# Kernel optimization log

Hardware: AMD Instinct MI355X
Metric: run time of the kernel (lower is better)

Reference implementation:

```python
import jax, jax.numpy as jnp
import numpy as np

# dims: B batch, N nodes, F in-feats, H time window, K Cheb order, G out-feats, C classes
B, N, F, H, K, G, C = 32, 16384, 1, 15, 25, 64, 6
E = N * 32  # edges


def setup_inputs() -> dict:
    key = jax.random.key(0)
    ks = jax.random.split(key, 8)
    x = jax.random.normal(ks[0], (B, N, F, H), jnp.float32)
    edge_src = jax.random.randint(ks[1], (E,), 0, N, jnp.int32)
    edge_dst = jax.random.randint(ks[2], (E,), 0, N, jnp.int32)
    # precomputed scaled-Laplacian edge weights (as in ChebConv norm)
    edge_weight = jax.random.uniform(ks[3], (E,), jnp.float32, minval=-0.1, maxval=0.1)
    W = jax.random.normal(ks[4], (K, H, F, G), jnp.float32) * 0.05   # Cheb time-conv weight
    b_conv = jnp.zeros((G,), jnp.float32)
    W_fc = jax.random.normal(ks[5], (C, N * G), jnp.float32) * 0.01  # torch Linear layout [out,in]
    b_fc = jnp.zeros((C,), jnp.float32)
    return dict(x=x, edge_weight=edge_weight, W=W, b_conv=b_conv,
                W_fc=W_fc, b_fc=b_fc, edge_src=edge_src, edge_dst=edge_dst)


def _spmm(edge_src, edge_dst, edge_weight, X):
    # sparse L @ X ; X: [N, D]  ->  y[i] = sum_{e: src=i} w_e * X[dst_e]
    return jax.ops.segment_sum(edge_weight[:, None] * X[edge_dst], edge_src, num_segments=N)


def reference(x, edge_weight, W, b_conv, W_fc, b_fc, edge_src, edge_dst):
    # Chebyshev recursion over the graph, joint contraction over time window and features
    X0 = jnp.transpose(x, (1, 0, 2, 3)).reshape(N, B * F * H)  # [N, B*F*H]

    def contract(Xk, Wk):
        # Xk: [N, B*F*H], Wk: [H, F, G] -> [B, N, G]
        return jnp.einsum('nbfh,hfg->bng', Xk.reshape(N, B, F, H), Wk)

    out = contract(X0, W[0])
    X1 = _spmm(edge_src, edge_dst, edge_weight, X0)
    out = out + contract(X1, W[1])
    Xkm2, Xkm1 = X0, X1
    for k in range(2, K):  # fixed K=25, structural loop
        Xk = 2.0 * _spmm(edge_src, edge_dst, edge_weight, Xkm1) - Xkm2
        out = out + contract(Xk, W[k])
        Xkm2, Xkm1 = Xkm1, Xk
    out = out + b_conv                         # [B, N, G]
    h = jax.nn.relu(out).reshape(B, N * G)     # x.view(B, -1)
    logits = h @ W_fc.T + b_fc                 # fc1
    return jax.nn.log_softmax(logits, axis=1)
```

## Files before the change

### kernel.cpp

```cpp
#include <hip/hip_runtime.h>
#include <hip/hip_bf16.h>
#include <math.h>

#define NN 16384
#define BB 32
#define HH 15
#define KK 25
#define GG 64
#define CC 6
#define EE (NN * 32)
#define NG ((size_t)NN * GG)
#define PSTRIDE 8192

typedef unsigned int u32;
typedef unsigned short u16;
typedef __attribute__((ext_vector_type(8))) short bf16x8;
typedef __attribute__((ext_vector_type(4))) float f32x4;
typedef __attribute__((ext_vector_type(4))) u32 u32x4;


__global__ void init_counts(int* __restrict__ cnt) {
    int t = blockIdx.x * 256 + threadIdx.x;
    if (t < NN) cnt[t] = 0;
}

__global__ void hist_kernel(const int* __restrict__ src, int* __restrict__ cnt) {
    int e = blockIdx.x * 256 + threadIdx.x;
    if (e < EE) atomicAdd(&cnt[src[e]], 1);
}

__global__ __launch_bounds__(1024) void scan_kernel(const int* __restrict__ cnt,
                                                    int* __restrict__ rowptr,
                                                    int* __restrict__ cursor) {
    __shared__ int sums[1024];
    int t = threadIdx.x;
    int base = t * 16;
    int local[16];
    int s = 0;
#pragma unroll
    for (int i = 0; i < 16; ++i) { local[i] = s; s += cnt[base + i]; }
    sums[t] = s;
    __syncthreads();
    for (int off = 1; off < 1024; off <<= 1) {
        int v = (t >= off) ? sums[t - off] : 0;
        __syncthreads();
        sums[t] += v;
        __syncthreads();
    }
    int prefix = (t == 0) ? 0 : sums[t - 1];
#pragma unroll
    for (int i = 0; i < 16; ++i) {
        int rp = prefix + local[i];
        rowptr[base + i] = rp;
        cursor[base + i] = rp;
    }
    if (t == 1023) rowptr[NN] = sums[1023];
}

__global__ void scatter_kernel(const int* __restrict__ src, const int* __restrict__ dst,
                               const float* __restrict__ w, int* __restrict__ cursor,
                               int* __restrict__ col, float* __restrict__ wgt) {
    int e = blockIdx.x * 256 + threadIdx.x;
    if (e < EE) {
        int pos = atomicAdd(&cursor[src[e]], 1);
        col[pos] = dst[e];
        wgt[pos] = w[e];
    }
}


__device__ __forceinline__ u16 f2bf(float f) {
    __hip_bfloat16 b = __float2bfloat16(f);
    return *reinterpret_cast<u16*>(&b);
}
__device__ __forceinline__ float bflo(u32 d) { return __uint_as_float(d << 16); }
__device__ __forceinline__ float bfhi(u32 d) { return __uint_as_float(d & 0xffff0000u); }


__global__ void prep_wbf(const float* __restrict__ W, u16* __restrict__ WbfT) {
    int t = blockIdx.x * 256 + threadIdx.x;
    if (t >= GG * 416) return;
    int g = t / 416;
    int f = t % 416;
    int k = f >> 4;
    int h = f & 15;
    float v = (k < KK && h < HH) ? W[(k * HH + h) * GG + g] : 0.f;
    WbfT[(size_t)g * 416 + f] = f2bf(v);
}


template<int BCH>
__global__ void transpose_bf(const float* __restrict__ x, u32* __restrict__ X0, int b0) {
    constexpr int CW = BCH * 8;
    int t = blockIdx.x * 256 + threadIdx.x;
    int n = t / CW;
    int j = t % CW;
    int bb = j >> 3;
    int h0 = (j & 7) * 2;
    const float* xb = x + ((size_t)(b0 + bb) * NN + n) * HH;
    float lo = xb[h0];
    float hi = (h0 + 1 < HH) ? xb[h0 + 1] : 0.f;
    X0[t] = (u32)f2bf(lo) | ((u32)f2bf(hi) << 16);
}


__global__ __launch_bounds__(256) void spmm_bf32(
    const int* __restrict__ rowptr, const int* __restrict__ col, const float* __restrict__ wgt,
    const u32* __restrict__ Xin, const u32* __restrict__ Xprev, u32* __restrict__ Xout,
    float alpha, float beta)
{
    int qc   = threadIdx.x >> 6;
    int lane = threadIdx.x & 63;
    int n = blockIdx.x;
    int e0 = rowptr[n], e1 = rowptr[n + 1];
    int grp = lane >> 4;
    int m16 = lane & 15;
    const u32* xq = Xin + (size_t)qc * 64 + (size_t)m16 * 4;

    float al[4] = {0.f,0.f,0.f,0.f}, ah[4] = {0.f,0.f,0.f,0.f};
    float bl[4] = {0.f,0.f,0.f,0.f}, bh[4] = {0.f,0.f,0.f,0.f};

    for (int base = e0; base < e1; base += 64) {
        int cnt = e1 - base;
        if (cnt > 64) cnt = 64;
        int cv = 0; float wv = 0.f;
        if (lane < cnt) { cv = col[base + lane]; wv = wgt[base + lane]; }
        int j = 0;
        for (; j + 8 <= cnt; j += 8) {
            int   iA = __shfl(cv, j + grp);
            float wA = __shfl(wv, j + grp);
            int   iB = __shfl(cv, j + 4 + grp);
            float wB = __shfl(wv, j + 4 + grp);
            u32x4 dA = *(const u32x4*)(xq + (size_t)iA * 256);
            u32x4 dB = *(const u32x4*)(xq + (size_t)iB * 256);
#pragma unroll
            for (int i = 0; i < 4; ++i) {
                al[i] = fmaf(wA, bflo(dA[i]), al[i]);
                ah[i] = fmaf(wA, bfhi(dA[i]), ah[i]);
                bl[i] = fmaf(wB, bflo(dB[i]), bl[i]);
                bh[i] = fmaf(wB, bfhi(dB[i]), bh[i]);
            }
        }
        for (; j < cnt; j += 4) {
            int   iA = __shfl(cv, j + grp);
            float wA = __shfl(wv, j + grp);
            u32x4 dA = *(const u32x4*)(xq + (size_t)iA * 256);
#pragma unroll
            for (int i = 0; i < 4; ++i) {
                al[i] = fmaf(wA, bflo(dA[i]), al[i]);
                ah[i] = fmaf(wA, bfhi(dA[i]), ah[i]);
            }
        }
    }

#pragma unroll
    for (int i = 0; i < 4; ++i) { al[i] += bl[i]; ah[i] += bh[i]; }
#pragma unroll
    for (int off = 16; off < 64; off <<= 1)
#pragma unroll
        for (int i = 0; i < 4; ++i) {
            al[i] += __shfl_xor(al[i], off);
            ah[i] += __shfl_xor(ah[i], off);
        }

    if (grp == 0) {
        size_t o = (size_t)n * 256 + (size_t)qc * 64 + (size_t)m16 * 4;
        u32x4 dp = {0,0,0,0};
        if (beta != 0.f) dp = *(const u32x4*)(Xprev + o);
        u32x4 r;
#pragma unroll
        for (int i = 0; i < 4; ++i) {
            float rl = alpha * al[i];
            float rh = alpha * ah[i];
            if (beta != 0.f) {
                rl = fmaf(beta, bflo(dp[i]), rl);
                rh = fmaf(beta, bfhi(dp[i]), rh);
            }
            r[i] = (u32)f2bf(rl) | ((u32)f2bf(rh) << 16);
        }
        *(u32x4*)(Xout + o) = r;
    }
}


__global__ __launch_bounds__(256) void spmm_bf8(
    const int* __restrict__ rowptr, const int* __restrict__ col, const float* __restrict__ wgt,
    const u32* __restrict__ Xin, const u32* __restrict__ Xprev, u32* __restrict__ Xout,
    float alpha, float beta)
{
    int sub  = threadIdx.x >> 6;
    int lane = threadIdx.x & 63;
    int n = blockIdx.x * 4 + sub;
    int e0 = rowptr[n], e1 = rowptr[n + 1];
    int grp = lane >> 4;
    int m16 = lane & 15;

    float al[4] = {0.f,0.f,0.f,0.f}, ah[4] = {0.f,0.f,0.f,0.f};
    float bl[4] = {0.f,0.f,0.f,0.f}, bh[4] = {0.f,0.f,0.f,0.f};

    for (int base = e0; base < e1; base += 64) {
        int cnt = e1 - base;
        if (cnt > 64) cnt = 64;
        int cv = 0; float wv = 0.f;
        if (lane < cnt) { cv = col[base + lane]; wv = wgt[base + lane]; }
        int j = 0;
        for (; j + 8 <= cnt; j += 8) {
            int   iA = __shfl(cv, j + grp);
            float wA = __shfl(wv, j + grp);
            int   iB = __shfl(cv, j + 4 + grp);
            float wB = __shfl(wv, j + 4 + grp);
            u32x4 dA = *(const u32x4*)(Xin + (size_t)iA * 64 + m16 * 4);
            u32x4 dB = *(const u32x4*)(Xin + (size_t)iB * 64 + m16 * 4);
#pragma unroll
            for (int i = 0; i < 4; ++i) {
                al[i] = fmaf(wA, bflo(dA[i]), al[i]);
                ah[i] = fmaf(wA, bfhi(dA[i]), ah[i]);
                bl[i] = fmaf(wB, bflo(dB[i]), bl[i]);
                bh[i] = fmaf(wB, bfhi(dB[i]), bh[i]);
            }
        }
        for (; j < cnt; j += 4) {
            int   iA = __shfl(cv, j + grp);
            float wA = __shfl(wv, j + grp);
            u32x4 dA = *(const u32x4*)(Xin + (size_t)iA * 64 + m16 * 4);
#pragma unroll
            for (int i = 0; i < 4; ++i) {
                al[i] = fmaf(wA, bflo(dA[i]), al[i]);
                ah[i] = fmaf(wA, bfhi(dA[i]), ah[i]);
            }
        }
    }

#pragma unroll
    for (int i = 0; i < 4; ++i) { al[i] += bl[i]; ah[i] += bh[i]; }
#pragma unroll
    for (int off = 16; off < 64; off <<= 1)
#pragma unroll
        for (int i = 0; i < 4; ++i) {
            al[i] += __shfl_xor(al[i], off);
            ah[i] += __shfl_xor(ah[i], off);
        }

    if (grp == 0) {
        size_t o = (size_t)n * 64 + (size_t)m16 * 4;
        u32x4 dp = {0,0,0,0};
        if (beta != 0.f) dp = *(const u32x4*)(Xprev + o);
        u32x4 r;
#pragma unroll
        for (int i = 0; i < 4; ++i) {
            float rl = alpha * al[i];
            float rh = alpha * ah[i];
            if (beta != 0.f) {
                rl = fmaf(beta, bflo(dp[i]), rl);
                rh = fmaf(beta, bfhi(dp[i]), rh);
            }
            r[i] = (u32)f2bf(rl) | ((u32)f2bf(rh) << 16);
        }
        *(u32x4*)(Xout + o) = r;
    }
}


__global__ __launch_bounds__(256) void spmm_bf4(
    const int* __restrict__ rowptr, const int* __restrict__ col, const float* __restrict__ wgt,
    const u32* __restrict__ Xin, const u32* __restrict__ Xprev, u32* __restrict__ Xout,
    float alpha, float beta)
{
    int sub  = threadIdx.x >> 6;
    int lane = threadIdx.x & 63;
    int n = blockIdx.x * 4 + sub;
    int e0 = rowptr[n], e1 = rowptr[n + 1];
    int grp = lane >> 3;
    int m8  = lane & 7;

    float al[4] = {0.f,0.f,0.f,0.f}, ah[4] = {0.f,0.f,0.f,0.f};
    float bl[4] = {0.f,0.f,0.f,0.f}, bh[4] = {0.f,0.f,0.f,0.f};

    for (int base = e0; base < e1; base += 64) {
        int cnt = e1 - base;
        if (cnt > 64) cnt = 64;
        int cv = 0; float wv = 0.f;
        if (lane < cnt) { cv = col[base + lane]; wv = wgt[base + lane]; }
        int j = 0;
        for (; j + 16 <= cnt; j += 16) {
            int   iA = __shfl(cv, j + grp);
            float wA = __shfl(wv, j + grp);
            int   iB = __shfl(cv, j + 8 + grp);
            float wB = __shfl(wv, j + 8 + grp);
            u32x4 dA = *(const u32x4*)(Xin + (size_t)iA * 32 + m8 * 4);
            u32x4 dB = *(const u32x4*)(Xin + (size_t)iB * 32 + m8 * 4);
#pragma unroll
            for (int i = 0; i < 4; ++i) {
                al[i] = fmaf(wA, bflo(dA[i]), al[i]);
                ah[i] = fmaf(wA, bfhi(dA[i]), ah[i]);
                bl[i] = fmaf(wB, bflo(dB[i]), bl[i]);
                bh[i] = fmaf(wB, bfhi(dB[i]), bh[i]);
            }
        }
        for (; j < cnt; j += 8) {
            int   iA = __shfl(cv, j + grp);
            float wA = __shfl(wv, j + grp);
            u32x4 dA = *(const u32x4*)(Xin + (size_t)iA * 32 + m8 * 4);
#pragma unroll
            for (int i = 0; i < 4; ++i) {
                al[i] = fmaf(wA, bflo(dA[i]), al[i]);
                ah[i] = fmaf(wA, bfhi(dA[i]), ah[i]);
            }
        }
    }

#pragma unroll
    for (int i = 0; i < 4; ++i) { al[i] += bl[i]; ah[i] += bh[i]; }
#pragma unroll
    for (int off = 8; off < 64; off <<= 1)
#pragma unroll
        for (int i = 0; i < 4; ++i) {
            al[i] += __shfl_xor(al[i], off);
            ah[i] += __shfl_xor(ah[i], off);
        }

    if (grp == 0) {
        size_t o = (size_t)n * 32 + (size_t)m8 * 4;
        u32x4 dp = {0,0,0,0};
        if (beta != 0.f) dp = *(const u32x4*)(Xprev + o);
        u32x4 r;
#pragma unroll
        for (int i = 0; i < 4; ++i) {
            float rl = alpha * al[i];
            float rh = alpha * ah[i];
            if (beta != 0.f) {
                rl = fmaf(beta, bflo(dp[i]), rl);
                rh = fmaf(beta, bfhi(dp[i]), rh);
            }
            r[i] = (u32)f2bf(rl) | ((u32)f2bf(rh) << 16);
        }
        *(u32x4*)(Xout + o) = r;
    }
}


template<int BCH>
__global__ __launch_bounds__(256) void spmm_bf(
    const int* __restrict__ rowptr, const int* __restrict__ col, const float* __restrict__ wgt,
    const u32* __restrict__ Xin, const u32* __restrict__ Xprev, u32* __restrict__ Xout,
    float alpha, float beta)
{
    constexpr int C  = BCH * 16;
    int sub  = threadIdx.x >> 6;
    int lane = threadIdx.x & 63;
    int n = blockIdx.x * 4 + sub;
    int e0 = rowptr[n], e1 = rowptr[n + 1];

    int c = lane;
    const u16* XinU  = (const u16*)Xin;
    const u16* XprevU= (const u16*)Xprev;
    u16* XoutU = (u16*)Xout;
    float a0=0.f,a1=0.f,a2=0.f,a3=0.f;
    bool act = (c < C);
    for (int base = e0; base < e1; base += 64) {
        int cnt = e1 - base;
        if (cnt > 64) cnt = 64;
        int cv = 0; float wv = 0.f;
        if (lane < cnt) { cv = col[base + lane]; wv = wgt[base + lane]; }
        int j = 0;
        for (; j + 4 <= cnt; j += 4) {
            int i0 = __builtin_amdgcn_readlane(cv, j);
            int i1 = __builtin_amdgcn_readlane(cv, j + 1);
            int i2 = __builtin_amdgcn_readlane(cv, j + 2);
            int i3 = __builtin_amdgcn_readlane(cv, j + 3);
            float w0 = __int_as_float(__builtin_amdgcn_readlane(__float_as_int(wv), j));
            float w1 = __int_as_float(__builtin_amdgcn_readlane(__float_as_int(wv), j + 1));
            float w2 = __int_as_float(__builtin_amdgcn_readlane(__float_as_int(wv), j + 2));
            float w3 = __int_as_float(__builtin_amdgcn_readlane(__float_as_int(wv), j + 3));
            if (act) {
                float x0 = __uint_as_float((u32)XinU[(size_t)i0 * C + c] << 16);
                float x1 = __uint_as_float((u32)XinU[(size_t)i1 * C + c] << 16);
                float x2 = __uint_as_float((u32)XinU[(size_t)i2 * C + c] << 16);
                float x3 = __uint_as_float((u32)XinU[(size_t)i3 * C + c] << 16);
                a0 = fmaf(w0, x0, a0);
                a1 = fmaf(w1, x1, a1);
                a2 = fmaf(w2, x2, a2);
                a3 = fmaf(w3, x3, a3);
            }
        }
        for (; j < cnt; ++j) {
            int i0 = __builtin_amdgcn_readlane(cv, j);
            float w0 = __int_as_float(__builtin_amdgcn_readlane(__float_as_int(wv), j));
            if (act) a0 = fmaf(w0, __uint_as_float((u32)XinU[(size_t)i0 * C + c] << 16), a0);
        }
    }
    if (act) {
        float r = alpha * ((a0 + a1) + (a2 + a3));
        size_t o = (size_t)n * C + c;
        if (beta != 0.f)
            r = fmaf(beta, __uint_as_float((u32)XprevU[o] << 16), r);
        XoutU[o] = f2bf(r);
    }
}


__global__ __launch_bounds__(256) void final4_32(
    const u32* __restrict__ Xall, const u16* __restrict__ WbfT,
    const float* __restrict__ b_conv, const float* __restrict__ Wfc,
    float* __restrict__ partials)
{
    constexpr int SLICE_DW = NN * 256;
    __shared__ float sred[2][32 * CC];
    int tid  = threadIdx.x;
    int wid  = tid >> 6;
    int lane = tid & 63;
    int q = lane >> 4;
    int m = lane & 15;
    int r0 = (blockIdx.x * 4 + wid) * 16;
    int r  = r0 + m;

    f32x4 acc0 = {0.f,0.f,0.f,0.f}, acc1 = {0.f,0.f,0.f,0.f};
    f32x4 acc2 = {0.f,0.f,0.f,0.f}, acc3 = {0.f,0.f,0.f,0.f};

    const u32* abase = Xall + (size_t)r * 8 + (size_t)(q & 1) * 4;
    const u16* bbase = WbfT + (size_t)m * 416 + q * 8;

#pragma unroll
    for (int s = 0; s < 13; ++s) {
        int ks = 2 * s + (q >> 1);
        bf16x8 af = {0,0,0,0,0,0,0,0};
        if (s < 12 || q < 2)
            af = *(const bf16x8*)(abase + (size_t)ks * SLICE_DW);
        bf16x8 bf0 = *(const bf16x8*)(bbase + (size_t)0 * 16 * 416 + s * 32);
        bf16x8 bf1 = *(const bf16x8*)(bbase + (size_t)1 * 16 * 416 + s * 32);
        bf16x8 bf2 = *(const bf16x8*)(bbase + (size_t)2 * 16 * 416 + s * 32);
        bf16x8 bf3 = *(const bf16x8*)(bbase + (size_t)3 * 16 * 416 + s * 32);
        acc0 = __builtin_amdgcn_mfma_f32_16x16x32_bf16(af, bf0, acc0, 0, 0, 0);
        acc1 = __builtin_amdgcn_mfma_f32_16x16x32_bf16(af, bf1, acc1, 0, 0, 0);
        acc2 = __builtin_amdgcn_mfma_f32_16x16x32_bf16(af, bf2, acc2, 0, 0, 0);
        acc3 = __builtin_amdgcn_mfma_f32_16x16x32_bf16(af, bf3, acc3, 0, 0, 0);
    }

    float part[4][CC];
#pragma unroll
    for (int i = 0; i < 4; ++i)
#pragma unroll
        for (int c = 0; c < CC; ++c) part[i][c] = 0.f;

#pragma unroll
    for (int gt = 0; gt < 4; ++gt) {
        f32x4 a = (gt == 0) ? acc0 : (gt == 1) ? acc1 : (gt == 2) ? acc2 : acc3;
        float bias = b_conv[gt * 16 + m];
#pragma unroll
        for (int i = 0; i < 4; ++i) {
            int rr = r0 + q * 4 + i;
            int nrow = rr >> 5;
            float hv = fmaxf(a[i] + bias, 0.f);
#pragma unroll
            for (int c = 0; c < CC; ++c)
                part[i][c] = fmaf(hv,
                    Wfc[(size_t)c * NG + (size_t)nrow * GG + gt * 16 + m], part[i][c]);
        }
    }

#pragma unroll
    for (int o = 1; o < 16; o <<= 1)
#pragma unroll
        for (int i = 0; i < 4; ++i)
#pragma unroll
            for (int c = 0; c < CC; ++c)
                part[i][c] += __shfl_xor(part[i][c], o);

    if (m == 0) {
        int node = wid >> 1;
        int bbb  = (wid & 1) * 16;
#pragma unroll
        for (int i = 0; i < 4; ++i)
#pragma unroll
            for (int c = 0; c < CC; ++c)
                sred[node][(bbb + q * 4 + i) * CC + c] = part[i][c];
    }
    __syncthreads();
    if (tid < 32 * CC) {
        float s2 = sred[0][tid] + sred[1][tid];
        int bb = tid / CC;
        int c  = tid % CC;
        partials[((size_t)bb * CC + c) * PSTRIDE + blockIdx.x] = s2;
    }
}


template<int BCH>
__global__ __launch_bounds__(256) void final4_t(
    const u32* __restrict__ Xall, const u16* __restrict__ WbfT,
    const float* __restrict__ b_conv, const float* __restrict__ Wfc,
    float* __restrict__ partials, int b0)
{
    constexpr int SLICE_DW = NN * BCH * 8;
    __shared__ float sred[4][BCH * CC];
    int tid  = threadIdx.x;
    int wid  = tid >> 6;
    int lane = tid & 63;
    int q = lane >> 4;
    int m = lane & 15;
    int r0 = (blockIdx.x * 4 + wid) * 16;
    int r  = r0 + m;

    f32x4 acc0 = {0.f,0.f,0.f,0.f}, acc1 = {0.f,0.f,0.f,0.f};
    f32x4 acc2 = {0.f,0.f,0.f,0.f}, acc3 = {0.f,0.f,0.f,0.f};

    const u32* abase = Xall + (size_t)r * 8 + (size_t)(q & 1) * 4;
    const u16* bbase = WbfT + (size_t)m * 416 + q * 8;

#pragma unroll
    for (int s = 0; s < 13; ++s) {
        int ks = 2 * s + (q >> 1);
        bf16x8 af = {0,0,0,0,0,0,0,0};
        if (s < 12 || q < 2)
            af = *(const bf16x8*)(abase + (size_t)ks * SLICE_DW);
        bf16x8 bf0 = *(const bf16x8*)(bbase + (size_t)0 * 16 * 416 + s * 32);
        bf16x8 bf1 = *(const bf16x8*)(bbase + (size_t)1 * 16 * 416 + s * 32);
        bf16x8 bf2 = *(const bf16x8*)(bbase + (size_t)2 * 16 * 416 + s * 32);
        bf16x8 bf3 = *(const bf16x8*)(bbase + (size_t)3 * 16 * 416 + s * 32);
        acc0 = __builtin_amdgcn_mfma_f32_16x16x32_bf16(af, bf0, acc0, 0, 0, 0);
        acc1 = __builtin_amdgcn_mfma_f32_16x16x32_bf16(af, bf1, acc1, 0, 0, 0);
        acc2 = __builtin_amdgcn_mfma_f32_16x16x32_bf16(af, bf2, acc2, 0, 0, 0);
        acc3 = __builtin_amdgcn_mfma_f32_16x16x32_bf16(af, bf3, acc3, 0, 0, 0);
    }

    float part[4][CC];
#pragma unroll
    for (int i = 0; i < 4; ++i)
#pragma unroll
        for (int c = 0; c < CC; ++c) part[i][c] = 0.f;

#pragma unroll
    for (int gt = 0; gt < 4; ++gt) {
        f32x4 a = (gt == 0) ? acc0 : (gt == 1) ? acc1 : (gt == 2) ? acc2 : acc3;
        float bias = b_conv[gt * 16 + m];
#pragma unroll
        for (int i = 0; i < 4; ++i) {
            int rr = r0 + q * 4 + i;
            int nrow = rr / BCH;
            float hv = fmaxf(a[i] + bias, 0.f);
#pragma unroll
            for (int c = 0; c < CC; ++c)
                part[i][c] = fmaf(hv,
                    Wfc[(size_t)c * NG + (size_t)nrow * GG + gt * 16 + m], part[i][c]);
        }
    }

#pragma unroll
    for (int o = 1; o < 16; o <<= 1)
#pragma unroll
        for (int i = 0; i < 4; ++i)
#pragma unroll
            for (int c = 0; c < CC; ++c)
                part[i][c] += __shfl_xor(part[i][c], o);

    if constexpr (BCH == 8) {
#pragma unroll
        for (int i = 0; i < 4; ++i)
#pragma unroll
            for (int c = 0; c < CC; ++c)
                part[i][c] += __shfl_xor(part[i][c], 32);
        if (m == 0 && q < 2) {
#pragma unroll
            for (int i = 0; i < 4; ++i)
#pragma unroll
                for (int c = 0; c < CC; ++c)
                    sred[wid][(q * 4 + i) * CC + c] = part[i][c];
        }
    } else {
#pragma unroll
        for (int o = 16; o < 64; o <<= 1)
#pragma unroll
            for (int i = 0; i < 4; ++i)
#pragma unroll
                for (int c = 0; c < CC; ++c)
                    part[i][c] += __shfl_xor(part[i][c], o);
        if (lane == 0) {
#pragma unroll
            for (int i = 0; i < 4; ++i)
#pragma unroll
                for (int c = 0; c < CC; ++c)
                    sred[wid][i * CC + c] = part[i][c];
        }
    }
    __syncthreads();
    if (tid < BCH * CC) {
        float s4 = sred[0][tid] + sred[1][tid] + sred[2][tid] + sred[3][tid];
        int bb = tid / CC;
        int c  = tid % CC;
        partials[((size_t)(b0 + bb) * CC + c) * PSTRIDE + blockIdx.x] = s4;
    }
}


template<int BCH>
__global__ __launch_bounds__(256) void final3_t(
    const u32* __restrict__ Xall, const float* __restrict__ W,
    const float* __restrict__ b_conv, const float* __restrict__ Wfc,
    float* __restrict__ partials, int b0)
{
    constexpr int CW = BCH * 8;
    __shared__ float sred[4][BCH * CC];
    int g   = threadIdx.x & 63;
    int nlu = __builtin_amdgcn_readfirstlane((int)threadIdx.x) >> 6;
    int n   = blockIdx.x * 4 + nlu;

    float acc[BCH];
#pragma unroll
    for (int bb = 0; bb < BCH; ++bb) acc[bb] = 0.f;

    for (int k = 0; k < KK; ++k) {
        const u32* __restrict__ xrow = Xall + ((size_t)k * NN + n) * CW;
        const float* __restrict__ Wk = W + k * (HH * GG);
        float wreg[HH];
#pragma unroll
        for (int h = 0; h < HH; ++h) wreg[h] = Wk[h * GG + g];
#pragma unroll
        for (int bb = 0; bb < BCH; ++bb) {
            float a = acc[bb];
#pragma unroll
            for (int p = 0; p < 8; ++p) {
                u32 d = xrow[bb * 8 + p];
                a = fmaf(bflo(d), wreg[2 * p], a);
                if (p < 7) a = fmaf(bfhi(d), wreg[2 * p + 1], a);
            }
            acc[bb] = a;
        }
    }

    float bias = b_conv[g];
    float wv[CC];
#pragma unroll
    for (int c = 0; c < CC; ++c)
        wv[c] = Wfc[(size_t)c * NG + (size_t)n * GG + g];

#pragma unroll
    for (int bb = 0; bb < BCH; ++bb) {
        float hv = fmaxf(acc[bb] + bias, 0.f);
#pragma unroll
        for (int c = 0; c < CC; ++c) {
            float s = hv * wv[c];
#pragma unroll
            for (int off = 1; off < 64; off <<= 1) s += __shfl_xor(s, off);
            if (g == 0) sred[nlu][bb * CC + c] = s;
        }
    }
    __syncthreads();
    if (threadIdx.x < BCH * CC) {
        float s = sred[0][threadIdx.x] + sred[1][threadIdx.x]
                + sred[2][threadIdx.x] + sred[3][threadIdx.x];
        int bb = threadIdx.x / CC;
        int c  = threadIdx.x % CC;
        partials[((size_t)(b0 + bb) * CC + c) * PSTRIDE + blockIdx.x] = s;
    }
}


__global__ __launch_bounds__(256) void reduce_logits(const float* __restrict__ partials,
                                                     float* __restrict__ logits, int nblk) {
    int idx = blockIdx.x;
    const float* p = partials + (size_t)idx * PSTRIDE;
    float s = 0.f;
    for (int i = threadIdx.x; i < nblk; i += 256) s += p[i];
#pragma unroll
    for (int off = 1; off < 64; off <<= 1) s += __shfl_xor(s, off);
    __shared__ float sr[4];
    if ((threadIdx.x & 63) == 0) sr[threadIdx.x >> 6] = s;
    __syncthreads();
    if (threadIdx.x == 0) logits[idx] = sr[0] + sr[1] + sr[2] + sr[3];
}


__global__ void lsm_kernel(const float* __restrict__ logits, const float* __restrict__ b_fc,
                           float* __restrict__ out) {
    int b = threadIdx.x;
    if (b >= BB) return;
    float v[CC];
    float m = -1e30f;
#pragma unroll
    for (int c = 0; c < CC; ++c) {
        v[c] = logits[b * CC + c] + b_fc[c];
        m = fmaxf(m, v[c]);
    }
    float s = 0.f;
#pragma unroll
    for (int c = 0; c < CC; ++c) s += expf(v[c] - m);
    float ls = m + logf(s);
#pragma unroll
    for (int c = 0; c < CC; ++c) out[b * CC + c] = v[c] - ls;
}

__global__ void sentinel_kernel(float* __restrict__ out) {
    int t = threadIdx.x;
    if (t < BB * CC) out[t] = -12345.f;
}


template<int BCH>
static void run_passes(const float* x, const float* W, const u16* WbfT,
                       const float* bconv, const float* Wfc,
                       const int* rowptr, const int* col, const float* wgt,
                       u32* Xall, float* partials, hipStream_t stream)
{
    constexpr int CW = BCH * 8;
    const size_t slice = (size_t)NN * CW;

    for (int p = 0; p < BB / BCH; ++p) {
        int b0 = p * BCH;
        transpose_bf<BCH><<<(NN * CW) / 256, 256, 0, stream>>>(x, Xall, b0);
        if constexpr (BCH == 32) {
            spmm_bf32<<<NN, 256, 0, stream>>>(
                rowptr, col, wgt, Xall, Xall, Xall + slice, 1.f, 0.f);
            for (int k = 2; k < KK; ++k) {
                spmm_bf32<<<NN, 256, 0, stream>>>(
                    rowptr, col, wgt,
                    Xall + (size_t)(k - 1) * slice,
                    Xall + (size_t)(k - 2) * slice,
                    Xall + (size_t)k * slice, 2.f, -1.f);
            }
            final4_32<<<NN * 32 / 64, 256, 0, stream>>>(Xall, WbfT, bconv, Wfc, partials);
        } else if constexpr (BCH == 8) {
            spmm_bf8<<<NN / 4, 256, 0, stream>>>(
                rowptr, col, wgt, Xall, Xall, Xall + slice, 1.f, 0.f);
            for (int k = 2; k < KK; ++k) {
                spmm_bf8<<<NN / 4, 256, 0, stream>>>(
                    rowptr, col, wgt,
                    Xall + (size_t)(k - 1) * slice,
                    Xall + (size_t)(k - 2) * slice,
                    Xall + (size_t)k * slice, 2.f, -1.f);
            }
            final4_t<8><<<NN * 8 / 64, 256, 0, stream>>>(Xall, WbfT, bconv, Wfc, partials, b0);
        } else if constexpr (BCH == 4) {
            spmm_bf4<<<NN / 4, 256, 0, stream>>>(
                rowptr, col, wgt, Xall, Xall, Xall + slice, 1.f, 0.f);
            for (int k = 2; k < KK; ++k) {
                spmm_bf4<<<NN / 4, 256, 0, stream>>>(
                    rowptr, col, wgt,
                    Xall + (size_t)(k - 1) * slice,
                    Xall + (size_t)(k - 2) * slice,
                    Xall + (size_t)k * slice, 2.f, -1.f);
            }
            final4_t<4><<<NN * 4 / 64, 256, 0, stream>>>(Xall, WbfT, bconv, Wfc, partials, b0);
        } else {
            spmm_bf<BCH><<<NN / 4, 256, 0, stream>>>(
                rowptr, col, wgt, Xall, Xall, Xall + slice, 1.f, 0.f);
            for (int k = 2; k < KK; ++k) {
                spmm_bf<BCH><<<NN / 4, 256, 0, stream>>>(
                    rowptr, col, wgt,
                    Xall + (size_t)(k - 1) * slice,
                    Xall + (size_t)(k - 2) * slice,
                    Xall + (size_t)k * slice, 2.f, -1.f);
            }
            final3_t<BCH><<<NN / 4, 256, 0, stream>>>(Xall, W, bconv, Wfc, partials, b0);
        }
    }
}


extern "C" void kernel_launch(void* const* d_in, const int* in_sizes, int n_in,
                              void* d_out, int out_size, void* d_ws, size_t ws_size,
                              hipStream_t stream) {
    const float* x     = (const float*)d_in[0];
    const float* ew    = (const float*)d_in[1];
    const float* W     = (const float*)d_in[2];
    const float* bconv = (const float*)d_in[3];
    const float* Wfc   = (const float*)d_in[4];
    const float* bfc   = (const float*)d_in[5];
    const int*   esrc  = (const int*)d_in[6];
    const int*   edst  = (const int*)d_in[7];
    float* out = (float*)d_out;

    char* ws = (char*)d_ws;
    size_t off = 0;
    auto alloc = [&](size_t bytes) -> void* {
        void* p = (void*)(ws + off);
        off = (off + bytes + 255) & ~(size_t)255;
        return p;
    };
    int*   rowptr   = (int*)  alloc((size_t)(NN + 1) * 4);
    int*   cursor   = (int*)  alloc((size_t)NN * 4);
    int*   cnt      = (int*)  alloc((size_t)NN * 4);
    int*   col      = (int*)  alloc((size_t)EE * 4);
    float* wgt      = (float*)alloc((size_t)EE * 4);
    float* logits   = (float*)alloc(256 * 4);
    u16*   WbfT     = (u16*)  alloc((size_t)GG * 416 * 2);
    float* partials = (float*)alloc((size_t)BB * CC * PSTRIDE * 4);
    size_t fixed = off;

    int BCH = 0;
    for (int b = 32; b >= 1; b >>= 1) {
        size_t need = fixed + (size_t)KK * NN * (size_t)b * 16 * 2;
        if (need <= ws_size) { BCH = b; break; }
        if (b == 32) b = 16;
    }
    if (BCH == 16) BCH = 8;
    if (BCH == 0) {
        sentinel_kernel<<<1, 256, 0, stream>>>(out);
        return;
    }
    u32* Xall = (u32*)(ws + fixed);

    init_counts<<<(NN + 255) / 256, 256, 0, stream>>>(cnt);
    hist_kernel<<<(EE + 255) / 256, 256, 0, stream>>>(esrc, cnt);
    scan_kernel<<<1, 1024, 0, stream>>>(cnt, rowptr, cursor);
    scatter_kernel<<<(EE + 255) / 256, 256, 0, stream>>>(esrc, edst, ew, cursor, col, wgt);
    prep_wbf<<<(GG * 416 + 255) / 256, 256, 0, stream>>>(W, WbfT);

    switch (BCH) {
        case 32: run_passes<32>(x, W, WbfT, bconv, Wfc, rowptr, col, wgt, Xall, partials, stream); break;
        case 8:  run_passes<8>(x, W, WbfT, bconv, Wfc, rowptr, col, wgt, Xall, partials, stream); break;
        case 4:  run_passes<4>(x, W, WbfT, bconv, Wfc, rowptr, col, wgt, Xall, partials, stream); break;
        case 2:  run_passes<2>(x, W, WbfT, bconv, Wfc, rowptr, col, wgt, Xall, partials, stream); break;
        default: run_passes<1>(x, W, WbfT, bconv, Wfc, rowptr, col, wgt, Xall, partials, stream); break;
    }

    int nblk = (BCH == 32) ? 8192 : (BCH == 8) ? 2048 : (BCH == 4) ? 1024 : (NN / 4);
    reduce_logits<<<BB * CC, 256, 0, stream>>>(partials, logits, nblk);
    lsm_kernel<<<1, 64, 0, stream>>>(logits, bfc, out);
}
```

Measured before the change: 1.650 ms.

## Split batch into 16-wide passes with two-node SpMM blocks and prefetched MFMA operands

Caps the batch chunk at 16 instead of 32, so the full 32-batch input is processed in two passes. Each Chebyshev slice is half as large, which shrinks the working set the random-neighbour gathers touch and should improve L2/LLC hit rates. The SpMM kernel now gives each 256-thread block two nodes, each handled by two wavefronts, with 256-byte rows. The final MFMA kernels preload all 13 A fragments into registers up front and declare occupancy launch bounds. The trade-off is twice as many kernel launches and twice the reading of the CSR col/weight arrays, plus higher register pressure in the final kernel.

```diff
diff --git a/kernel.cpp b/kernel.cpp
--- a/kernel.cpp
+++ b/kernel.cpp
@@ -104,18 +104,19 @@
 }
 
 
-__global__ __launch_bounds__(256) void spmm_bf32(
+__global__ __launch_bounds__(256) void spmm_bf16k(
     const int* __restrict__ rowptr, const int* __restrict__ col, const float* __restrict__ wgt,
     const u32* __restrict__ Xin, const u32* __restrict__ Xprev, u32* __restrict__ Xout,
     float alpha, float beta)
 {
-    int qc   = threadIdx.x >> 6;
+    int sub  = threadIdx.x >> 6;
     int lane = threadIdx.x & 63;
-    int n = blockIdx.x;
+    int n    = blockIdx.x * 2 + (sub >> 1);
+    int half = sub & 1;
     int e0 = rowptr[n], e1 = rowptr[n + 1];
     int grp = lane >> 4;
     int m16 = lane & 15;
-    const u32* xq = Xin + (size_t)qc * 64 + (size_t)m16 * 4;
+    const u32* xq = Xin + (size_t)half * 64 + (size_t)m16 * 4;
 
     float al[4] = {0.f,0.f,0.f,0.f}, ah[4] = {0.f,0.f,0.f,0.f};
     float bl[4] = {0.f,0.f,0.f,0.f}, bh[4] = {0.f,0.f,0.f,0.f};
@@ -131,8 +132,8 @@
             float wA = __shfl(wv, j + grp);
             int   iB = __shfl(cv, j + 4 + grp);
             float wB = __shfl(wv, j + 4 + grp);
-            u32x4 dA = *(const u32x4*)(xq + (size_t)iA * 256);
-            u32x4 dB = *(const u32x4*)(xq + (size_t)iB * 256);
+            u32x4 dA = *(const u32x4*)(xq + (size_t)iA * 128);
+            u32x4 dB = *(const u32x4*)(xq + (size_t)iB * 128);
 #pragma unroll
             for (int i = 0; i < 4; ++i) {
                 al[i] = fmaf(wA, bflo(dA[i]), al[i]);
@@ -144,7 +145,7 @@
         for (; j < cnt; j += 4) {
             int   iA = __shfl(cv, j + grp);
             float wA = __shfl(wv, j + grp);
-            u32x4 dA = *(const u32x4*)(xq + (size_t)iA * 256);
+            u32x4 dA = *(const u32x4*)(xq + (size_t)iA * 128);
 #pragma unroll
             for (int i = 0; i < 4; ++i) {
                 al[i] = fmaf(wA, bflo(dA[i]), al[i]);
@@ -164,7 +165,7 @@
         }
 
     if (grp == 0) {
-        size_t o = (size_t)n * 256 + (size_t)qc * 64 + (size_t)m16 * 4;
+        size_t o = (size_t)n * 128 + (size_t)half * 64 + (size_t)m16 * 4;
         u32x4 dp = {0,0,0,0};
         if (beta != 0.f) dp = *(const u32x4*)(Xprev + o);
         u32x4 r;
@@ -399,7 +400,128 @@
 }
 
 
-__global__ __launch_bounds__(256) void final4_32(
+template<int BCH>
+__global__ __launch_bounds__(256, 4) void final4_t(
+    const u32* __restrict__ Xall, const u16* __restrict__ WbfT,
+    const float* __restrict__ b_conv, const float* __restrict__ Wfc,
+    float* __restrict__ partials, int b0)
+{
+    constexpr int SLICE_DW = NN * BCH * 8;
+    __shared__ float sred[4][BCH * CC];
+    int tid  = threadIdx.x;
+    int wid  = tid >> 6;
+    int lane = tid & 63;
+    int q = lane >> 4;
+    int m = lane & 15;
+    int r0 = (blockIdx.x * 4 + wid) * 16;
+    int r  = r0 + m;
+
+    const u32* abase = Xall + (size_t)r * 8 + (size_t)(q & 1) * 4;
+    const u16* bbase = WbfT + (size_t)m * 416 + q * 8;
+
+    bf16x8 af[13];
+#pragma unroll
+    for (int s = 0; s < 13; ++s) {
+        int ks = 2 * s + (q >> 1);
+        bf16x8 t = {0,0,0,0,0,0,0,0};
+        if (s < 12 || q < 2)
+            t = *(const bf16x8*)(abase + (size_t)ks * SLICE_DW);
+        af[s] = t;
+    }
+
+    f32x4 acc0 = {0.f,0.f,0.f,0.f}, acc1 = {0.f,0.f,0.f,0.f};
+    f32x4 acc2 = {0.f,0.f,0.f,0.f}, acc3 = {0.f,0.f,0.f,0.f};
+
+#pragma unroll
+    for (int s = 0; s < 13; ++s) {
+        bf16x8 bf0 = *(const bf16x8*)(bbase + (size_t)0 * 16 * 416 + s * 32);
+        bf16x8 bf1 = *(const bf16x8*)(bbase + (size_t)1 * 16 * 416 + s * 32);
+        bf16x8 bf2 = *(const bf16x8*)(bbase + (size_t)2 * 16 * 416 + s * 32);
+        bf16x8 bf3 = *(const bf16x8*)(bbase + (size_t)3 * 16 * 416 + s * 32);
+        acc0 = __builtin_amdgcn_mfma_f32_16x16x32_bf16(af[s], bf0, acc0, 0, 0, 0);
+        acc1 = __builtin_amdgcn_mfma_f32_16x16x32_bf16(af[s], bf1, acc1, 0, 0, 0);
+        acc2 = __builtin_amdgcn_mfma_f32_16x16x32_bf16(af[s], bf2, acc2, 0, 0, 0);
+        acc3 = __builtin_amdgcn_mfma_f32_16x16x32_bf16(af[s], bf3, acc3, 0, 0, 0);
+    }
+
+    float part[4][CC];
+#pragma unroll
+    for (int i = 0; i < 4; ++i)
+#pragma unroll
+        for (int c = 0; c < CC; ++c) part[i][c] = 0.f;
+
+#pragma unroll
+    for (int gt = 0; gt < 4; ++gt) {
+        f32x4 a = (gt == 0) ? acc0 : (gt == 1) ? acc1 : (gt == 2) ? acc2 : acc3;
+        float bias = b_conv[gt * 16 + m];
+#pragma unroll
+        for (int i = 0; i < 4; ++i) {
+            int rr = r0 + q * 4 + i;
+            int nrow = rr / BCH;
+            float hv = fmaxf(a[i] + bias, 0.f);
+#pragma unroll
+            for (int c = 0; c < CC; ++c)
+                part[i][c] = fmaf(hv,
+                    Wfc[(size_t)c * NG + (size_t)nrow * GG + gt * 16 + m], part[i][c]);
+        }
+    }
+
+#pragma unroll
+    for (int o = 1; o < 16; o <<= 1)
+#pragma unroll
+        for (int i = 0; i < 4; ++i)
+#pragma unroll
+            for (int c = 0; c < CC; ++c)
+                part[i][c] += __shfl_xor(part[i][c], o);
+
+    if constexpr (BCH == 16) {
+        if (m == 0) {
+#pragma unroll
+            for (int i = 0; i < 4; ++i)
+#pragma unroll
+                for (int c = 0; c < CC; ++c)
+                    sred[wid][(q * 4 + i) * CC + c] = part[i][c];
+        }
+    } else if constexpr (BCH == 8) {
+#pragma unroll
+        for (int i = 0; i < 4; ++i)
+#pragma unroll
+            for (int c = 0; c < CC; ++c)
+                part[i][c] += __shfl_xor(part[i][c], 32);
+        if (m == 0 && q < 2) {
+#pragma unroll
+            for (int i = 0; i < 4; ++i)
+#pragma unroll
+                for (int c = 0; c < CC; ++c)
+                    sred[wid][(q * 4 + i) * CC + c] = part[i][c];
+        }
+    } else {
+#pragma unroll
+        for (int o = 16; o < 64; o <<= 1)
+#pragma unroll
+            for (int i = 0; i < 4; ++i)
+#pragma unroll
+                for (int c = 0; c < CC; ++c)
+                    part[i][c] += __shfl_xor(part[i][c], o);
+        if (lane == 0) {
+#pragma unroll
+            for (int i = 0; i < 4; ++i)
+#pragma unroll
+                for (int c = 0; c < CC; ++c)
+                    sred[wid][i * CC + c] = part[i][c];
+        }
+    }
+    __syncthreads();
+    if (tid < BCH * CC) {
+        float s4 = sred[0][tid] + sred[1][tid] + sred[2][tid] + sred[3][tid];
+        int bb = tid / CC;
+        int c  = tid % CC;
+        partials[((size_t)(b0 + bb) * CC + c) * PSTRIDE + blockIdx.x] = s4;
+    }
+}
+
+
+__global__ __launch_bounds__(256, 4) void final4_32(
     const u32* __restrict__ Xall, const u16* __restrict__ WbfT,
     const float* __restrict__ b_conv, const float* __restrict__ Wfc,
     float* __restrict__ partials)
@@ -414,26 +536,32 @@
     int r0 = (blockIdx.x * 4 + wid) * 16;
     int r  = r0 + m;
 
+    const u32* abase = Xall + (size_t)r * 8 + (size_t)(q & 1) * 4;
+    const u16* bbase = WbfT + (size_t)m * 416 + q * 8;
+
+    bf16x8 af[13];
+#pragma unroll
+    for (int s = 0; s < 13; ++s) {
+        int ks = 2 * s + (q >> 1);
+        bf16x8 t = {0,0,0,0,0,0,0,0};
+        if (s < 12 || q < 2)
+            t = *(const bf16x8*)(abase + (size_t)ks * SLICE_DW);
+        af[s] = t;
+    }
+
     f32x4 acc0 = {0.f,0.f,0.f,0.f}, acc1 = {0.f,0.f,0.f,0.f};
     f32x4 acc2 = {0.f,0.f,0.f,0.f}, acc3 = {0.f,0.f,0.f,0.f};
 
-    const u32* abase = Xall + (size_t)r * 8 + (size_t)(q & 1) * 4;
-    const u16* bbase = WbfT + (size_t)m * 416 + q * 8;
-
 #pragma unroll
     for (int s = 0; s < 13; ++s) {
-        int ks = 2 * s + (q >> 1);
-        bf16x8 af = {0,0,0,0,0,0,0,0};
-        if (s < 12 || q < 2)
-            af = *(const bf16x8*)(abase + (size_t)ks * SLICE_DW);
         bf16x8 bf0 = *(const bf16x8*)(bbase + (size_t)0 * 16 * 416 + s * 32);
         bf16x8 bf1 = *(const bf16x8*)(bbase + (size_t)1 * 16 * 416 + s * 32);
         bf16x8 bf2 = *(const bf16x8*)(bbase + (size_t)2 * 16 * 416 + s * 32);
         bf16x8 bf3 = *(const bf16x8*)(bbase + (size_t)3 * 16 * 416 + s * 32);
-        acc0 = __builtin_amdgcn_mfma_f32_16x16x32_bf16(af, bf0, acc0, 0, 0, 0);
-        acc1 = __builtin_amdgcn_mfma_f32_16x16x32_bf16(af, bf1, acc1, 0, 0, 0);
-        acc2 = __builtin_amdgcn_mfma_f32_16x16x32_bf16(af, bf2, acc2, 0, 0, 0);
-        acc3 = __builtin_amdgcn_mfma_f32_16x16x32_bf16(af, bf3, acc3, 0, 0, 0);
+        acc0 = __builtin_amdgcn_mfma_f32_16x16x32_bf16(af[s], bf0, acc0, 0, 0, 0);
+        acc1 = __builtin_amdgcn_mfma_f32_16x16x32_bf16(af[s], bf1, acc1, 0, 0, 0);
+        acc2 = __builtin_amdgcn_mfma_f32_16x16x32_bf16(af[s], bf2, acc2, 0, 0, 0);
+        acc3 = __builtin_amdgcn_mfma_f32_16x16x32_bf16(af[s], bf3, acc3, 0, 0, 0);
     }
 
     float part[4][CC];
@@ -481,113 +609,6 @@
         int bb = tid / CC;
         int c  = tid % CC;
         partials[((size_t)bb * CC + c) * PSTRIDE + blockIdx.x] = s2;
-    }
-}
-
-
-template<int BCH>
-__global__ __launch_bounds__(256) void final4_t(
-    const u32* __restrict__ Xall, const u16* __restrict__ WbfT,
-    const float* __restrict__ b_conv, const float* __restrict__ Wfc,
-    float* __restrict__ partials, int b0)
-{
-    constexpr int SLICE_DW = NN * BCH * 8;
-    __shared__ float sred[4][BCH * CC];
-    int tid  = threadIdx.x;
-    int wid  = tid >> 6;
-    int lane = tid & 63;
-    int q = lane >> 4;
-    int m = lane & 15;
-    int r0 = (blockIdx.x * 4 + wid) * 16;
-    int r  = r0 + m;
-
-    f32x4 acc0 = {0.f,0.f,0.f,0.f}, acc1 = {0.f,0.f,0.f,0.f};
-    f32x4 acc2 = {0.f,0.f,0.f,0.f}, acc3 = {0.f,0.f,0.f,0.f};
-
-    const u32* abase = Xall + (size_t)r * 8 + (size_t)(q & 1) * 4;
-    const u16* bbase = WbfT + (size_t)m * 416 + q * 8;
-
-#pragma unroll
-    for (int s = 0; s < 13; ++s) {
-        int ks = 2 * s + (q >> 1);
-        bf16x8 af = {0,0,0,0,0,0,0,0};
-        if (s < 12 || q < 2)
-            af = *(const bf16x8*)(abase + (size_t)ks * SLICE_DW);
-        bf16x8 bf0 = *(const bf16x8*)(bbase + (size_t)0 * 16 * 416 + s * 32);
-        bf16x8 bf1 = *(const bf16x8*)(bbase + (size_t)1 * 16 * 416 + s * 32);
-        bf16x8 bf2 = *(const bf16x8*)(bbase + (size_t)2 * 16 * 416 + s * 32);
-        bf16x8 bf3 = *(const bf16x8*)(bbase + (size_t)3 * 16 * 416 + s * 32);
-        acc0 = __builtin_amdgcn_mfma_f32_16x16x32_bf16(af, bf0, acc0, 0, 0, 0);
-        acc1 = __builtin_amdgcn_mfma_f32_16x16x32_bf16(af, bf1, acc1, 0, 0, 0);
-        acc2 = __builtin_amdgcn_mfma_f32_16x16x32_bf16(af, bf2, acc2, 0, 0, 0);
-        acc3 = __builtin_amdgcn_mfma_f32_16x16x32_bf16(af, bf3, acc3, 0, 0, 0);
-    }
-
-    float part[4][CC];
-#pragma unroll
-    for (int i = 0; i < 4; ++i)
-#pragma unroll
-        for (int c = 0; c < CC; ++c) part[i][c] = 0.f;
-
-#pragma unroll
-    for (int gt = 0; gt < 4; ++gt) {
-        f32x4 a = (gt == 0) ? acc0 : (gt == 1) ? acc1 : (gt == 2) ? acc2 : acc3;
-        float bias = b_conv[gt * 16 + m];
-#pragma unroll
-        for (int i = 0; i < 4; ++i) {
-            int rr = r0 + q * 4 + i;
-            int nrow = rr / BCH;
-            float hv = fmaxf(a[i] + bias, 0.f);
-#pragma unroll
-            for (int c = 0; c < CC; ++c)
-                part[i][c] = fmaf(hv,
-                    Wfc[(size_t)c * NG + (size_t)nrow * GG + gt * 16 + m], part[i][c]);
-        }
-    }
-
-#pragma unroll
-    for (int o = 1; o < 16; o <<= 1)
-#pragma unroll
-        for (int i = 0; i < 4; ++i)
-#pragma unroll
-            for (int c = 0; c < CC; ++c)
-                part[i][c] += __shfl_xor(part[i][c], o);
-
-    if constexpr (BCH == 8) {
-#pragma unroll
-        for (int i = 0; i < 4; ++i)
-#pragma unroll
-            for (int c = 0; c < CC; ++c)
-                part[i][c] += __shfl_xor(part[i][c], 32);
-        if (m == 0 && q < 2) {
-#pragma unroll
-            for (int i = 0; i < 4; ++i)
-#pragma unroll
-                for (int c = 0; c < CC; ++c)
-                    sred[wid][(q * 4 + i) * CC + c] = part[i][c];
-        }
-    } else {
-#pragma unroll
-        for (int o = 16; o < 64; o <<= 1)
-#pragma unroll
-            for (int i = 0; i < 4; ++i)
-#pragma unroll
-                for (int c = 0; c < CC; ++c)
-                    part[i][c] += __shfl_xor(part[i][c], o);
-        if (lane == 0) {
-#pragma unroll
-            for (int i = 0; i < 4; ++i)
-#pragma unroll
-                for (int c = 0; c < CC; ++c)
-                    sred[wid][i * CC + c] = part[i][c];
-        }
-    }
-    __syncthreads();
-    if (tid < BCH * CC) {
-        float s4 = sred[0][tid] + sred[1][tid] + sred[2][tid] + sred[3][tid];
-        int bb = tid / CC;
-        int c  = tid % CC;
-        partials[((size_t)(b0 + bb) * CC + c) * PSTRIDE + blockIdx.x] = s4;
     }
 }
 
@@ -708,16 +729,19 @@
         int b0 = p * BCH;
         transpose_bf<BCH><<<(NN * CW) / 256, 256, 0, stream>>>(x, Xall, b0);
         if constexpr (BCH == 32) {
-            spmm_bf32<<<NN, 256, 0, stream>>>(
+            spmm_bf16k<<<NN / 2, 256, 0, stream>>>(
+                rowptr, col, wgt, Xall, Xall, Xall + slice, 1.f, 0.f);
+        } else if constexpr (BCH == 16) {
+            spmm_bf16k<<<NN / 2, 256, 0, stream>>>(
                 rowptr, col, wgt, Xall, Xall, Xall + slice, 1.f, 0.f);
             for (int k = 2; k < KK; ++k) {
-                spmm_bf32<<<NN, 256, 0, stream>>>(
+                spmm_bf16k<<<NN / 2, 256, 0, stream>>>(
                     rowptr, col, wgt,
                     Xall + (size_t)(k - 1) * slice,
                     Xall + (size_t)(k - 2) * slice,
                     Xall + (size_t)k * slice, 2.f, -1.f);
             }
-            final4_32<<<NN * 32 / 64, 256, 0, stream>>>(Xall, WbfT, bconv, Wfc, partials);
+            final4_t<16><<<NN * 16 / 64, 256, 0, stream>>>(Xall, WbfT, bconv, Wfc, partials, b0);
         } else if constexpr (BCH == 8) {
             spmm_bf8<<<NN / 4, 256, 0, stream>>>(
                 rowptr, col, wgt, Xall, Xall, Xall + slice, 1.f, 0.f);
@@ -786,13 +810,13 @@
     float* partials = (float*)alloc((size_t)BB * CC * PSTRIDE * 4);
     size_t fixed = off;
 
+    const int tiers[6] = {16, 8, 4, 2, 1, 0};
     int BCH = 0;
-    for (int b = 32; b >= 1; b >>= 1) {
+    for (int ti = 0; ti < 5; ++ti) {
+        int b = tiers[ti];
         size_t need = fixed + (size_t)KK * NN * (size_t)b * 16 * 2;
         if (need <= ws_size) { BCH = b; break; }
-        if (b == 32) b = 16;
-    }
-    if (BCH == 16) BCH = 8;
+    }
     if (BCH == 0) {
         sentinel_kernel<<<1, 256, 0, stream>>>(out);
         return;
@@ -806,14 +830,14 @@
     prep_wbf<<<(GG * 416 + 255) / 256, 256, 0, stream>>>(W, WbfT);
 
     switch (BCH) {
-        case 32: run_passes<32>(x, W, WbfT, bconv, Wfc, rowptr, col, wgt, Xall, partials, stream); break;
+        case 16: run_passes<16>(x, W, WbfT, bconv, Wfc, rowptr, col, wgt, Xall, partials, stream); break;
         case 8:  run_passes<8>(x, W, WbfT, bconv, Wfc, rowptr, col, wgt, Xall, partials, stream); break;
         case 4:  run_passes<4>(x, W, WbfT, bconv, Wfc, rowptr, col, wgt, Xall, partials, stream); break;
         case 2:  run_passes<2>(x, W, WbfT, bconv, Wfc, rowptr, col, wgt, Xall, partials, stream); break;
         default: run_passes<1>(x, W, WbfT, bconv, Wfc, rowptr, col, wgt, Xall, partials, stream); break;
     }
 
-    int nblk = (BCH == 32) ? 8192 : (BCH == 8) ? 2048 : (BCH == 4) ? 1024 : (NN / 4);
+    int nblk = (BCH == 16) ? 4096 : (BCH == 8) ? 2048 : (BCH == 4) ? 1024 : (NN / 4);
     reduce_logits<<<BB * CC, 256, 0, stream>>>(partials, logits, nblk);
     lsm_kernel<<<1, 64, 0, stream>>>(logits, bfc, out);
 }
```

Measured after the change: 1.696 ms. 1.03x slower.
